# Kernel tuning notes

Hardware: AMD Instinct MI355X
Metric: run time of the kernel (lower is better)

The kernel has to match this reference:

```python
import jax, jax.numpy as jnp
import numpy as np

B, S, T, D, N, V = 16, 4, 1000, 256, 8192, 50000
EPS = 2.220446049250313e-16  # sys.float_info.epsilon


def setup_inputs() -> dict:
    key = jax.random.key(0)
    ks = jax.random.split(key, 10)
    spks = jax.random.normal(ks[0], (B, S, T, D), jnp.float32)   # frame-level speaker vectors
    ys = jax.random.uniform(ks[1], (B, T, S), jnp.float32)        # predictions (unused in math)
    ts = jax.random.uniform(ks[2], (B, T, S), jnp.float32)        # soft targets / weights
    ss = jax.random.randint(ks[3], (B, S), 0, N)                  # candidate index per speaker
    sigmas = jnp.argsort(jax.random.uniform(ks[4], (B, S)), axis=1)  # per-sample permutation
    ns = jax.random.randint(ks[5], (B, N), 0, V)                  # candidate speaker ids
    ilens = jax.random.randint(ks[6], (B,), T // 2, T + 1)        # valid frame counts
    table = jax.random.normal(ks[7], (V, D), jnp.float32)         # nn.Embedding weight
    alpha = jax.random.uniform(ks[8], (), jnp.float32) + 0.5
    beta = jax.random.uniform(ks[9], (), jnp.float32) + 0.5
    return {"spks": spks, "ys": ys, "ts": ts, "ss": ss, "sigmas": sigmas,
            "ns": ns, "ilens": ilens, "table": table, "alpha": alpha, "beta": beta}


def reference(spks, ys, ts, ss, sigmas, ns, ilens, table, alpha, beta):
    # frame validity mask [B,T]
    mask = (jnp.arange(T)[None, :] < ilens[:, None]).astype(spks.dtype)
    # per-frame L2 normalize speaker vectors: [B,S,T,D]
    nspk = spks / jnp.linalg.norm(spks, axis=-1, keepdims=True)
    # weights w[b,s,t] = ts[b, t, sigma[b,s]]
    w_raw = jnp.take_along_axis(ts, sigmas[:, None, :], axis=2)  # [B,T,S]
    w_raw = jnp.transpose(w_raw, (0, 2, 1))                      # [B,S,T]
    w = w_raw * mask[:, None, :]
    # weighted average over valid frames, then normalize: [B,S,D]
    wavg = jnp.einsum('bst,bstd->bsd', w, nspk)
    e = wavg / jnp.linalg.norm(wavg, axis=-1, keepdims=True)
    # gather + normalize candidate embeddings: [B,N,D]
    emb = table[ns]
    emb = emb / jnp.linalg.norm(emb, axis=-1, keepdims=True)
    # squared euclidean distance between unit vectors: dist^2 = 2 - 2 cos
    dist2 = jnp.maximum(2.0 - 2.0 * jnp.einsum('bsd,bnd->bsn', e, emb), 0.0)
    d = jnp.maximum(alpha, EPS) * dist2 + beta                   # [B,S,N]
    logp = jax.nn.log_softmax(-d, axis=-1)
    idx = jnp.take_along_axis(ss, sigmas, axis=1)                # s[sigma[spkid]] -> [B,S]
    loss_bs = -jnp.take_along_axis(logp, idx[:, :, None], axis=-1)[..., 0]  # [B,S]
    # speaker active iff sum of rounded targets over valid frames > 0
    active = jnp.sum(jnp.round(w_raw) * mask[:, None, :], axis=-1) > 0
    loss_bs = jnp.where(active, loss_bs, 0.0)
    return jnp.mean(loss_bs)
```

## Files before the change

kernel.cpp:

```cpp
#include <hip/hip_runtime.h>
#include <math.h>

#define B_ 16
#define S_ 4
#define T_ 1000
#define D_ 256
#define N_ 8192
#define V_ 50000

constexpr int NC1 = 20;
constexpr int TC1 = (T_ + NC1 - 1) / NC1;
constexpr int CPB3 = 256;
constexpr int NC3 = N_ / CPB3;

constexpr size_t OFF_W   = 0;
constexpr size_t OFF_CNT = OFF_W   + (size_t)B_*S_*NC1*D_;
constexpr size_t OFF_E   = OFF_CNT + (size_t)B_*S_*NC1;
constexpr size_t OFF_IDX = OFF_E   + (size_t)B_*S_*D_;
constexpr size_t OFF_ACT = OFF_IDX + (size_t)B_*S_;
constexpr size_t OFF_DT  = OFF_ACT + (size_t)B_*S_;
constexpr size_t OFF_SE  = OFF_DT  + (size_t)B_*S_;
constexpr size_t WS_FLOATS = OFF_SE + (size_t)B_*NC3*S_;

__global__ __launch_bounds__(256) void k1_frames(
    const float* __restrict__ spks, const float* __restrict__ ts,
    const int* __restrict__ sigmas, const int* __restrict__ ilens,
    float* __restrict__ Wp, float* __restrict__ Cp)
{
    const int blk   = blockIdx.x;
    const int bs    = blk / NC1;
    const int chunk = blk % NC1;
    const int b = bs / S_, s = bs % S_;
    const int sig  = sigmas[b * S_ + s];
    const int ilen = ilens[b];
    const int t0 = chunk * TC1;
    int t1 = t0 + TC1; if (t1 > T_) t1 = T_; if (t1 > ilen) t1 = ilen;

    const int wid  = threadIdx.x >> 6;
    const int lane = threadIdx.x & 63;

    float4 acc = make_float4(0.f, 0.f, 0.f, 0.f);
    float  cnt = 0.f;
    const float* base = spks + (size_t)bs * T_ * D_;

    for (int t = t0 + wid; t < t1; t += 4) {
        float4 v = *(const float4*)(base + (size_t)t * D_ + lane * 4);
        float n2 = v.x * v.x + v.y * v.y + v.z * v.z + v.w * v.w;
        #pragma unroll
        for (int o = 32; o >= 1; o >>= 1) n2 += __shfl_xor(n2, o, 64);
        const float w = ts[(b * T_ + t) * S_ + sig];
        const float scale = w / sqrtf(n2);
        acc.x += v.x * scale; acc.y += v.y * scale;
        acc.z += v.z * scale; acc.w += v.w * scale;
        if (lane == 0) cnt += rintf(w);
    }

    __shared__ float sacc[4][D_];
    __shared__ float scnt[4];
    sacc[wid][lane * 4 + 0] = acc.x;
    sacc[wid][lane * 4 + 1] = acc.y;
    sacc[wid][lane * 4 + 2] = acc.z;
    sacc[wid][lane * 4 + 3] = acc.w;
    if (lane == 0) scnt[wid] = cnt;
    __syncthreads();

    const int d = threadIdx.x;
    const float sum = sacc[0][d] + sacc[1][d] + sacc[2][d] + sacc[3][d];
    Wp[((size_t)bs * NC1 + chunk) * D_ + d] = sum;
    if (threadIdx.x == 0)
        Cp[(size_t)bs * NC1 + chunk] = scnt[0] + scnt[1] + scnt[2] + scnt[3];
}

__global__ __launch_bounds__(256) void k2_evec(
    const float* __restrict__ Wp, const float* __restrict__ Cp,
    const int* __restrict__ ss, const int* __restrict__ sigmas,
    float* __restrict__ E, int* __restrict__ IDX, float* __restrict__ ACT)
{
    const int bs = blockIdx.x;
    const int d  = threadIdx.x;
    float sum = 0.f;
    for (int c = 0; c < NC1; ++c) sum += Wp[((size_t)bs * NC1 + c) * D_ + d];

    float n2 = sum * sum;
    #pragma unroll
    for (int o = 32; o >= 1; o >>= 1) n2 += __shfl_xor(n2, o, 64);
    __shared__ float wsum[4];
    if ((threadIdx.x & 63) == 0) wsum[threadIdx.x >> 6] = n2;
    __syncthreads();
    const float tot = wsum[0] + wsum[1] + wsum[2] + wsum[3];

    E[(size_t)bs * D_ + d] = sum / sqrtf(tot);

    if (threadIdx.x == 0) {
        float c = 0.f;
        for (int i = 0; i < NC1; ++i) c += Cp[(size_t)bs * NC1 + i];
        ACT[bs] = c;
        const int b = bs / S_, s = bs % S_;
        IDX[bs] = ss[b * S_ + sigmas[b * S_ + s]];
    }
}

__global__ __launch_bounds__(256) void k3_dist(
    const float* __restrict__ table, const int* __restrict__ ns,
    const float* __restrict__ E, const int* __restrict__ IDX,
    const float* __restrict__ alpha_p, const float* __restrict__ beta_p,
    float* __restrict__ DT, float* __restrict__ SE)
{
    const int b     = blockIdx.x / NC3;
    const int chunk = blockIdx.x % NC3;
    const int wid  = threadIdx.x >> 6;
    const int lane = threadIdx.x & 63;

    __shared__ float e_s[S_ * D_];
    for (int i = threadIdx.x; i < S_ * D_; i += 256)
        e_s[i] = E[(size_t)b * S_ * D_ + i];
    __syncthreads();

    const float alpha = fmaxf(alpha_p[0], 2.220446049250313e-16f);
    const float beta  = beta_p[0];
    int tgt[S_];
    #pragma unroll
    for (int s2 = 0; s2 < S_; ++s2) tgt[s2] = IDX[b * S_ + s2];

    const int n  = chunk * CPB3 + threadIdx.x;
    const int id = ns[b * N_ + n];
    const float* __restrict__ row = table + (size_t)id * D_;

    float n2 = 0.f;
    float dp[S_] = {0.f, 0.f, 0.f, 0.f};
    #pragma unroll 4
    for (int d = 0; d < D_; d += 4) {
        const float4 v = *(const float4*)(row + d);
        n2 += v.x * v.x + v.y * v.y + v.z * v.z + v.w * v.w;
        #pragma unroll
        for (int s2 = 0; s2 < S_; ++s2) {
            const float4 e4 = *(const float4*)(e_s + s2 * D_ + d);
            dp[s2] += e4.x * v.x + e4.y * v.y + e4.z * v.z + e4.w * v.w;
        }
    }

    const float invn = 1.f / sqrtf(n2);
    float se[S_];
    #pragma unroll
    for (int s2 = 0; s2 < S_; ++s2) {
        const float cosv  = dp[s2] * invn;
        const float dist2 = fmaxf(2.f - 2.f * cosv, 0.f);
        const float dd    = alpha * dist2 + beta;
        se[s2] = expf(-dd);
        if (n == tgt[s2]) DT[b * S_ + s2] = dd;
    }

    #pragma unroll
    for (int o = 32; o >= 1; o >>= 1) {
        #pragma unroll
        for (int s2 = 0; s2 < S_; ++s2) se[s2] += __shfl_xor(se[s2], o, 64);
    }
    __shared__ float sse[4][S_];
    if (lane == 0) {
        #pragma unroll
        for (int s2 = 0; s2 < S_; ++s2) sse[wid][s2] = se[s2];
    }
    __syncthreads();
    if (threadIdx.x < S_) {
        const int s2 = threadIdx.x;
        SE[((size_t)b * NC3 + chunk) * S_ + s2] =
            sse[0][s2] + sse[1][s2] + sse[2][s2] + sse[3][s2];
    }
}

__global__ __launch_bounds__(64) void k4_final(
    const float* __restrict__ SE, const float* __restrict__ DT,
    const float* __restrict__ ACT, float* __restrict__ out)
{
    const int bs = threadIdx.x;
    const int b = bs / S_, s = bs % S_;
    double sum = 0.0;
    for (int c = 0; c < NC3; ++c) sum += (double)SE[((size_t)b * NC3 + c) * S_ + s];
    float loss = DT[bs] + (float)log(sum);
    if (!(ACT[bs] > 0.f)) loss = 0.f;
    float v = loss;
    #pragma unroll
    for (int o = 32; o >= 1; o >>= 1) v += __shfl_xor(v, o, 64);
    if (bs == 0) out[0] = v / 64.f;
}

extern "C" void kernel_launch(void* const* d_in, const int* in_sizes, int n_in,
                              void* d_out, int out_size, void* d_ws, size_t ws_size,
                              hipStream_t stream)
{
    const float* spks   = (const float*)d_in[0];
    const float* ts     = (const float*)d_in[2];
    const int*   ss     = (const int*)  d_in[3];
    const int*   sigmas = (const int*)  d_in[4];
    const int*   ns     = (const int*)  d_in[5];
    const int*   ilens  = (const int*)  d_in[6];
    const float* table  = (const float*)d_in[7];
    const float* alpha  = (const float*)d_in[8];
    const float* beta   = (const float*)d_in[9];
    float* out = (float*)d_out;

    float* ws = (float*)d_ws;
    float* Wp  = ws + OFF_W;
    float* Cp  = ws + OFF_CNT;
    float* E   = ws + OFF_E;
    int*   IDX = (int*)(ws + OFF_IDX);
    float* ACT = ws + OFF_ACT;
    float* DT  = ws + OFF_DT;
    float* SE  = ws + OFF_SE;

    k1_frames<<<B_ * S_ * NC1, 256, 0, stream>>>(spks, ts, sigmas, ilens, Wp, Cp);
    k2_evec  <<<B_ * S_,       256, 0, stream>>>(Wp, Cp, ss, sigmas, E, IDX, ACT);
    k3_dist  <<<B_ * NC3,      256, 0, stream>>>(table, ns, E, IDX, alpha, beta, DT, SE);
    k4_final <<<1,              64, 0, stream>>>(SE, DT, ACT, out);
}
```

Measured before the change: 47.44 us.

## Split each candidate row across four threads in distance kernel

The distance kernel now gives each embedding row to four threads, each handling a 64-wide slice of D, instead of one thread per row. Each block covers 64 candidates instead of 256, so there are four times as many blocks. Partial norms and dot products are combined with intra-quad shuffles. The shared E vectors are stored in padded 68-float rows to avoid LDS bank conflicts with the new access pattern. This raises memory-level parallelism and reads rows more coalesced across the gather, at the cost of extra shuffles and more partial sums for the final kernel to reduce.

Measured after the change: 60.49 us. +27.5%, slower.

```diff
diff --git a/kernel.cpp b/kernel.cpp
--- a/kernel.cpp
+++ b/kernel.cpp
@@ -10,7 +10,7 @@
 
 constexpr int NC1 = 20;
 constexpr int TC1 = (T_ + NC1 - 1) / NC1;
-constexpr int CPB3 = 256;
+constexpr int CPB3 = 64;
 constexpr int NC3 = N_ / CPB3;
 
 constexpr size_t OFF_W   = 0;
@@ -110,10 +110,14 @@
     const int chunk = blockIdx.x % NC3;
     const int wid  = threadIdx.x >> 6;
     const int lane = threadIdx.x & 63;
-
-    __shared__ float e_s[S_ * D_];
-    for (int i = threadIdx.x; i < S_ * D_; i += 256)
-        e_s[i] = E[(size_t)b * S_ * D_ + i];
+    const int q    = threadIdx.x & 3;
+    const int cloc = threadIdx.x >> 2;
+
+    __shared__ float e_s[S_ * 4 * 68];
+    for (int i = threadIdx.x; i < S_ * D_; i += 256) {
+        const int s2 = i >> 8, d = i & 255;
+        e_s[(s2 * 4 + (d >> 6)) * 68 + (d & 63)] = E[(size_t)b * S_ * D_ + i];
+    }
     __syncthreads();
 
     const float alpha = fmaxf(alpha_p[0], 2.220446049250313e-16f);
@@ -122,21 +126,28 @@
     #pragma unroll
     for (int s2 = 0; s2 < S_; ++s2) tgt[s2] = IDX[b * S_ + s2];
 
-    const int n  = chunk * CPB3 + threadIdx.x;
+    const int n  = chunk * CPB3 + cloc;
     const int id = ns[b * N_ + n];
-    const float* __restrict__ row = table + (size_t)id * D_;
+    const float* __restrict__ row = table + (size_t)id * D_ + q * 64;
 
     float n2 = 0.f;
     float dp[S_] = {0.f, 0.f, 0.f, 0.f};
     #pragma unroll 4
-    for (int d = 0; d < D_; d += 4) {
-        const float4 v = *(const float4*)(row + d);
+    for (int i = 0; i < 16; ++i) {
+        const float4 v = *(const float4*)(row + i * 4);
         n2 += v.x * v.x + v.y * v.y + v.z * v.z + v.w * v.w;
         #pragma unroll
         for (int s2 = 0; s2 < S_; ++s2) {
-            const float4 e4 = *(const float4*)(e_s + s2 * D_ + d);
+            const float4 e4 = *(const float4*)(e_s + (s2 * 4 + q) * 68 + i * 4);
             dp[s2] += e4.x * v.x + e4.y * v.y + e4.z * v.z + e4.w * v.w;
         }
+    }
+
+    #pragma unroll
+    for (int o = 1; o <= 2; o <<= 1) {
+        n2 += __shfl_xor(n2, o, 64);
+        #pragma unroll
+        for (int s2 = 0; s2 < S_; ++s2) dp[s2] += __shfl_xor(dp[s2], o, 64);
     }
 
     const float invn = 1.f / sqrtf(n2);
@@ -146,12 +157,12 @@
         const float cosv  = dp[s2] * invn;
         const float dist2 = fmaxf(2.f - 2.f * cosv, 0.f);
         const float dd    = alpha * dist2 + beta;
-        se[s2] = expf(-dd);
-        if (n == tgt[s2]) DT[b * S_ + s2] = dd;
-    }
-
-    #pragma unroll
-    for (int o = 32; o >= 1; o >>= 1) {
+        se[s2] = (q == 0) ? expf(-dd) : 0.f;
+        if (q == 0 && n == tgt[s2]) DT[b * S_ + s2] = dd;
+    }
+
+    #pragma unroll
+    for (int o = 4; o <= 32; o <<= 1) {
         #pragma unroll
         for (int s2 = 0; s2 < S_; ++s2) se[s2] += __shfl_xor(se[s2], o, 64);
     }
```

## Precompute normalized dot products of the whole embedding table against all speaker vectors

Applied to the files above, without the earlier changes.

Adds a tiled kernel that streams the full embedding table once. It computes each row's normalized dot product with all 64 speaker vectors into a V×64 workspace buffer. A light kernel then gathers four cosines per candidate and does the softmax partial sums, replacing the per-candidate gather of full 1 KB table rows. This trades the repeated random row reads (131k candidates against 50k rows) for one sequential table pass plus a 12.8 MB intermediate write. The new path is used only when the workspace is large enough, otherwise the old gather kernel runs.

After: 124.8 us. 163% more time.

```diff
diff --git a/kernel.cpp b/kernel.cpp
--- a/kernel.cpp
+++ b/kernel.cpp
@@ -10,17 +10,24 @@
 
 constexpr int NC1 = 20;
 constexpr int TC1 = (T_ + NC1 - 1) / NC1;
-constexpr int CPB3 = 256;
-constexpr int NC3 = N_ / CPB3;
+constexpr int NCSE = 32;
+constexpr int CPSE = N_ / NCSE;
+
+constexpr int GR   = 64;
+constexpr int GDCH = 32;
+constexpr int GPAD = GDCH + 4;
+constexpr int GNB  = (V_ + GR - 1) / GR;
 
 constexpr size_t OFF_W   = 0;
-constexpr size_t OFF_CNT = OFF_W   + (size_t)B_*S_*NC1*D_;
-constexpr size_t OFF_E   = OFF_CNT + (size_t)B_*S_*NC1;
-constexpr size_t OFF_IDX = OFF_E   + (size_t)B_*S_*D_;
-constexpr size_t OFF_ACT = OFF_IDX + (size_t)B_*S_;
-constexpr size_t OFF_DT  = OFF_ACT + (size_t)B_*S_;
-constexpr size_t OFF_SE  = OFF_DT  + (size_t)B_*S_;
-constexpr size_t WS_FLOATS = OFF_SE + (size_t)B_*NC3*S_;
+constexpr size_t OFF_CNT = OFF_W   + (size_t)64*NC1*D_;
+constexpr size_t OFF_E   = OFF_CNT + (size_t)64*NC1;
+constexpr size_t OFF_IDX = OFF_E   + (size_t)64*D_;
+constexpr size_t OFF_ACT = OFF_IDX + 64;
+constexpr size_t OFF_DT  = OFF_ACT + 64;
+constexpr size_t OFF_SE  = OFF_DT  + 64;
+constexpr size_t OFF_DOT = OFF_SE  + (size_t)B_*NCSE*S_;
+constexpr size_t WS_SMALL_FLOATS = OFF_DOT;
+constexpr size_t WS_FULL_FLOATS  = OFF_DOT + (size_t)V_*64;
 
 __global__ __launch_bounds__(256) void k1_frames(
     const float* __restrict__ spks, const float* __restrict__ ts,
@@ -100,14 +107,139 @@
     }
 }
 
-__global__ __launch_bounds__(256) void k3_dist(
+__global__ __launch_bounds__(256) void kG_dots(
+    const float* __restrict__ table, const float* __restrict__ E,
+    float* __restrict__ dots)
+{
+    const int v0  = blockIdx.x * GR;
+    const int tid = threadIdx.x;
+
+    __shared__ float rowsL[GR][GPAD];
+    __shared__ float eL[64][GPAD];
+    __shared__ float n2L[GR];
+
+    const int rg = tid & 15;
+    const int cg = tid >> 4;
+    const int sr = tid >> 3;
+    const int ssl = tid & 7;
+
+    float acc[4][4];
+    float n2[4];
+    #pragma unroll
+    for (int i = 0; i < 4; ++i) {
+        n2[i] = 0.f;
+        #pragma unroll
+        for (int j = 0; j < 4; ++j) acc[i][j] = 0.f;
+    }
+
+    for (int ch = 0; ch < D_ / GDCH; ++ch) {
+        const int d0 = ch * GDCH;
+        if (ch) __syncthreads();
+        #pragma unroll
+        for (int h = 0; h < 2; ++h) {
+            const int r  = sr + 32 * h;
+            const int gv = v0 + r;
+            float4 v = make_float4(0.f, 0.f, 0.f, 0.f);
+            if (gv < V_) v = *(const float4*)(table + (size_t)gv * D_ + d0 + ssl * 4);
+            *(float4*)&rowsL[r][ssl * 4] = v;
+            *(float4*)&eL[r][ssl * 4] =
+                *(const float4*)(E + (size_t)r * D_ + d0 + ssl * 4);
+        }
+        __syncthreads();
+
+        #pragma unroll
+        for (int dk = 0; dk < GDCH; dk += 4) {
+            float4 rv[4], cv[4];
+            #pragma unroll
+            for (int ri = 0; ri < 4; ++ri)
+                rv[ri] = *(const float4*)&rowsL[rg + 16 * ri][dk];
+            #pragma unroll
+            for (int ci = 0; ci < 4; ++ci)
+                cv[ci] = *(const float4*)&eL[cg + 16 * ci][dk];
+            #pragma unroll
+            for (int ri = 0; ri < 4; ++ri) {
+                #pragma unroll
+                for (int ci = 0; ci < 4; ++ci)
+                    acc[ri][ci] += rv[ri].x * cv[ci].x + rv[ri].y * cv[ci].y
+                                 + rv[ri].z * cv[ci].z + rv[ri].w * cv[ci].w;
+                if (cg == 0)
+                    n2[ri] += rv[ri].x * rv[ri].x + rv[ri].y * rv[ri].y
+                            + rv[ri].z * rv[ri].z + rv[ri].w * rv[ri].w;
+            }
+        }
+    }
+
+    if (cg == 0) {
+        #pragma unroll
+        for (int ri = 0; ri < 4; ++ri) n2L[rg + 16 * ri] = n2[ri];
+    }
+    __syncthreads();
+
+    #pragma unroll
+    for (int ri = 0; ri < 4; ++ri) {
+        const int v = v0 + rg + 16 * ri;
+        if (v < V_) {
+            const float rinv = 1.f / sqrtf(n2L[rg + 16 * ri]);
+            #pragma unroll
+            for (int ci = 0; ci < 4; ++ci)
+                dots[(size_t)v * 64 + cg + 16 * ci] = acc[ri][ci] * rinv;
+        }
+    }
+}
+
+__global__ __launch_bounds__(256) void k3b_soft(
+    const float* __restrict__ dots, const int* __restrict__ ns,
+    const int* __restrict__ IDX,
+    const float* __restrict__ alpha_p, const float* __restrict__ beta_p,
+    float* __restrict__ DT, float* __restrict__ SE)
+{
+    const int b     = blockIdx.x / NCSE;
+    const int chunk = blockIdx.x % NCSE;
+    const int tid   = threadIdx.x;
+    const int wid   = tid >> 6;
+    const int lane  = tid & 63;
+
+    const float alpha = fmaxf(alpha_p[0], 2.220446049250313e-16f);
+    const float beta  = beta_p[0];
+
+    const int n  = chunk * CPSE + tid;
+    const int id = ns[b * N_ + n];
+    const float4 c4 = *(const float4*)(dots + (size_t)id * 64 + b * 4);
+    const float cos4[4] = {c4.x, c4.y, c4.z, c4.w};
+
+    float se[S_];
+    #pragma unroll
+    for (int s2 = 0; s2 < S_; ++s2) {
+        const float dist2 = fmaxf(2.f - 2.f * cos4[s2], 0.f);
+        const float dd    = alpha * dist2 + beta;
+        se[s2] = expf(-dd);
+        if (n == IDX[b * S_ + s2]) DT[b * S_ + s2] = dd;
+    }
+
+    #pragma unroll
+    for (int o = 1; o <= 32; o <<= 1) {
+        #pragma unroll
+        for (int s2 = 0; s2 < S_; ++s2) se[s2] += __shfl_xor(se[s2], o, 64);
+    }
+    __shared__ float sse[4][S_];
+    if (lane == 0) {
+        #pragma unroll
+        for (int s2 = 0; s2 < S_; ++s2) sse[wid][s2] = se[s2];
+    }
+    __syncthreads();
+    if (tid < S_)
+        SE[((size_t)b * NCSE + chunk) * S_ + tid] =
+            sse[0][tid] + sse[1][tid] + sse[2][tid] + sse[3][tid];
+}
+
+__global__ __launch_bounds__(256) void k3_gather(
     const float* __restrict__ table, const int* __restrict__ ns,
     const float* __restrict__ E, const int* __restrict__ IDX,
     const float* __restrict__ alpha_p, const float* __restrict__ beta_p,
     float* __restrict__ DT, float* __restrict__ SE)
 {
-    const int b     = blockIdx.x / NC3;
-    const int chunk = blockIdx.x % NC3;
+    const int b     = blockIdx.x / NCSE;
+    const int chunk = blockIdx.x % NCSE;
     const int wid  = threadIdx.x >> 6;
     const int lane = threadIdx.x & 63;
 
@@ -122,7 +254,7 @@
     #pragma unroll
     for (int s2 = 0; s2 < S_; ++s2) tgt[s2] = IDX[b * S_ + s2];
 
-    const int n  = chunk * CPB3 + threadIdx.x;
+    const int n  = chunk * CPSE + threadIdx.x;
     const int id = ns[b * N_ + n];
     const float* __restrict__ row = table + (size_t)id * D_;
 
@@ -151,7 +283,7 @@
     }
 
     #pragma unroll
-    for (int o = 32; o >= 1; o >>= 1) {
+    for (int o = 1; o <= 32; o <<= 1) {
         #pragma unroll
         for (int s2 = 0; s2 < S_; ++s2) se[s2] += __shfl_xor(se[s2], o, 64);
     }
@@ -161,11 +293,10 @@
         for (int s2 = 0; s2 < S_; ++s2) sse[wid][s2] = se[s2];
     }
     __syncthreads();
-    if (threadIdx.x < S_) {
-        const int s2 = threadIdx.x;
-        SE[((size_t)b * NC3 + chunk) * S_ + s2] =
-            sse[0][s2] + sse[1][s2] + sse[2][s2] + sse[3][s2];
-    }
+    if (threadIdx.x < S_)
+        SE[((size_t)b * NCSE + chunk) * S_ + threadIdx.x] =
+            sse[0][threadIdx.x] + sse[1][threadIdx.x] +
+            sse[2][threadIdx.x] + sse[3][threadIdx.x];
 }
 
 __global__ __launch_bounds__(64) void k4_final(
@@ -175,7 +306,7 @@
     const int bs = threadIdx.x;
     const int b = bs / S_, s = bs % S_;
     double sum = 0.0;
-    for (int c = 0; c < NC3; ++c) sum += (double)SE[((size_t)b * NC3 + c) * S_ + s];
+    for (int c = 0; c < NCSE; ++c) sum += (double)SE[((size_t)b * NCSE + c) * S_ + s];
     float loss = DT[bs] + (float)log(sum);
     if (!(ACT[bs] > 0.f)) loss = 0.f;
     float v = loss;
@@ -207,9 +338,16 @@
     float* ACT = ws + OFF_ACT;
     float* DT  = ws + OFF_DT;
     float* SE  = ws + OFF_SE;
-
-    k1_frames<<<B_ * S_ * NC1, 256, 0, stream>>>(spks, ts, sigmas, ilens, Wp, Cp);
-    k2_evec  <<<B_ * S_,       256, 0, stream>>>(Wp, Cp, ss, sigmas, E, IDX, ACT);
-    k3_dist  <<<B_ * NC3,      256, 0, stream>>>(table, ns, E, IDX, alpha, beta, DT, SE);
-    k4_final <<<1,              64, 0, stream>>>(SE, DT, ACT, out);
-}
+    float* DOT = ws + OFF_DOT;
+
+    k1_frames<<<64 * NC1, 256, 0, stream>>>(spks, ts, sigmas, ilens, Wp, Cp);
+    k2_evec  <<<64,       256, 0, stream>>>(Wp, Cp, ss, sigmas, E, IDX, ACT);
+
+    if (ws_size >= WS_FULL_FLOATS * sizeof(float)) {
+        kG_dots <<<GNB,        256, 0, stream>>>(table, E, DOT);
+        k3b_soft<<<B_ * NCSE,  256, 0, stream>>>(DOT, ns, IDX, alpha, beta, DT, SE);
+    } else {
+        k3_gather<<<B_ * NCSE, 256, 0, stream>>>(table, ns, E, IDX, alpha, beta, DT, SE);
+    }
+    k4_final <<<1, 64, 0, stream>>>(SE, DT, ACT, out);
+}
```
